# Performance work log

Measured on AMD Instinct MI355X. Metric: run time of the kernel, lower is better.

The kernel has to match this reference:

```python
import jax, jax.numpy as jnp
import numpy as np
import math

D = 1024
H = 16
HD = D // H  # 64
SCALE = math.sqrt(HD)


def setup_inputs() -> dict:
    key = jax.random.key(0)
    ks = jax.random.split(key, 4)
    B, S = 2, 2048
    x = jax.random.normal(ks[0], (B, S, D), dtype=jnp.float32)
    attention_mask = jnp.zeros((B, S), dtype=jnp.float32)  # additive mask
    w_attn = jax.random.normal(ks[1], (D, 3 * D), dtype=jnp.float32) * (1.0 / math.sqrt(D))
    b_attn = jnp.zeros((3 * D,), dtype=jnp.float32)
    w_proj = jax.random.normal(ks[2], (D, D), dtype=jnp.float32) * (1.0 / math.sqrt(D))
    b_proj = jnp.zeros((D,), dtype=jnp.float32)
    return {"x": x, "attention_mask": attention_mask, "w_attn": w_attn,
            "b_attn": b_attn, "w_proj": w_proj, "b_proj": b_proj}


def reference(x, attention_mask, w_attn, b_attn, w_proj, b_proj):
    B, S, _ = x.shape
    qkv = x @ w_attn + b_attn                      # [B,S,3D]
    q, k, v = jnp.split(qkv, 3, axis=-1)           # each [B,S,D]
    # split heads -> [B,H,S,HD]
    sh = lambda t: t.reshape(B, S, H, HD).transpose(0, 2, 1, 3)
    q, k, v = sh(q), sh(k), sh(v)
    scores = jnp.einsum('bhqd,bhkd->bhqk', q, k) / SCALE   # [B,H,S,S]
    scores = scores + attention_mask[:, None, None, :]      # additive mask [B,1,1,S]
    attn = jax.nn.softmax(scores, axis=-1)                  # dropout disabled (eval)
    out = jnp.einsum('bhqk,bhkd->bhqd', attn, v)            # [B,H,S,HD]
    out = out.transpose(0, 2, 1, 3).reshape(B, S, D)        # merge heads
    out = out @ w_proj + b_proj                              # resid dropout disabled
    return out
```

## Files before the change

### kernel.cpp

```cpp
#include <hip/hip_runtime.h>
#include <math.h>

#define B_  2
#define S_  2048
#define D_  1024
#define H_  16
#define HD_ 64
#define BS_ (B_ * S_)

typedef float f32x4 __attribute__((ext_vector_type(4)));
typedef int   i32x4 __attribute__((ext_vector_type(4)));

__device__ __forceinline__ float bf2f(unsigned short u) {
    union { unsigned int i; float f; } c; c.i = ((unsigned int)u) << 16; return c.f;
}
__device__ __forceinline__ unsigned short f2bf(float f) {
    union { float f; unsigned int i; } c; c.f = f;
    unsigned int r = c.i + 0x7FFFu + ((c.i >> 16) & 1u);
    return (unsigned short)(r >> 16);
}
__device__ __forceinline__ unsigned int cvtpk_bf16(float lo, float hi) {
    unsigned int r;
    asm volatile("v_cvt_pk_bf16_f32 %0, %1, %2" : "=v"(r) : "v"(lo), "v"(hi));
    return r;
}
__device__ __forceinline__ void gl_lds16(const void* g, void* l) {
    __builtin_amdgcn_global_load_lds((const __attribute__((address_space(1))) void*)g,
                                     (__attribute__((address_space(3))) void*)l, 16, 0, 0);
}
__device__ __forceinline__ void mfma_bf16(f32x4& d, i32x4 a, i32x4 b) {
    asm volatile("v_mfma_f32_16x16x32_bf16 %0, %1, %2, %0" : "+v"(d) : "v"(a), "v"(b));
}

__global__ __launch_bounds__(256) void convert_f32_bf16(
    const float* __restrict__ in, unsigned short* __restrict__ out, int n)
{
    const int i = (blockIdx.x * 256 + threadIdx.x) * 8;
    if (i >= n) return;
    const float4 a = *reinterpret_cast<const float4*>(in + i);
    const float4 b = *reinterpret_cast<const float4*>(in + i + 4);
    ushort4 u0 = make_ushort4(f2bf(a.x), f2bf(a.y), f2bf(a.z), f2bf(a.w));
    ushort4 u1 = make_ushort4(f2bf(b.x), f2bf(b.y), f2bf(b.z), f2bf(b.w));
    *reinterpret_cast<ushort4*>(out + i)     = u0;
    *reinterpret_cast<ushort4*>(out + i + 4) = u1;
}

__global__ __launch_bounds__(256) void transpose_cvt(
    const float* __restrict__ W, unsigned short* __restrict__ Wt, int K, int N)
{
    __shared__ float t[32][33];
    const int n0 = blockIdx.x * 32, k0 = blockIdx.y * 32;
    const int tx = threadIdx.x & 31, ty = threadIdx.x >> 5;
#pragma unroll
    for (int r = 0; r < 32; r += 8)
        t[ty + r][tx] = W[(size_t)(k0 + ty + r) * N + n0 + tx];
    __syncthreads();
#pragma unroll
    for (int r = 0; r < 32; r += 8)
        Wt[(size_t)(n0 + ty + r) * K + k0 + tx] = f2bf(t[tx][ty + r]);
}

template <typename OutT>
__global__ __launch_bounds__(256) void gemm_bt_bf16(
    const unsigned short* __restrict__ A,
    const unsigned short* __restrict__ Bt,
    const float* __restrict__ bias,
    OutT* __restrict__ C, int M, int N, int K)
{
    __shared__ alignas(16) unsigned short As[4096];
    __shared__ alignas(16) unsigned short Bs[4096];

    const int tid  = threadIdx.x;
    const int wave = tid >> 6;
    const int l    = tid & 63;
    const int g    = l >> 4;
    const int r    = l & 15;
    const int wr   = wave >> 1, wc = wave & 1;
    const int row0 = blockIdx.y * 128;
    const int col0 = blockIdx.x * 128;

    const size_t aoff0 = (size_t)(row0 +   0 + l) * K + wave * 8;
    const size_t aoff1 = (size_t)(row0 +  64 + l) * K + wave * 8;
    const size_t boff0 = (size_t)(col0 +   0 + l) * K + wave * 8;
    const size_t boff1 = (size_t)(col0 +  64 + l) * K + wave * 8;

    f32x4 acc[4][4];
#pragma unroll
    for (int mi = 0; mi < 4; ++mi)
#pragma unroll
        for (int ni = 0; ni < 4; ++ni) acc[mi][ni] = (f32x4)0.f;

    for (int kt = 0; kt < K; kt += 32) {
        __syncthreads();
        gl_lds16(A  + aoff0 + kt, As + wave * 1024);
        gl_lds16(A  + aoff1 + kt, As + wave * 1024 + 512);
        gl_lds16(Bt + boff0 + kt, Bs + wave * 1024);
        gl_lds16(Bt + boff1 + kt, Bs + wave * 1024 + 512);
        __syncthreads();

        const unsigned short* Ab = As + g * 1024;
        const unsigned short* Bb = Bs + g * 1024;
        i32x4 af[4], bf[4];
#pragma unroll
        for (int mi = 0; mi < 4; ++mi)
            af[mi] = *reinterpret_cast<const i32x4*>(Ab + (wr * 64 + mi * 16 + r) * 8);
#pragma unroll
        for (int ni = 0; ni < 4; ++ni)
            bf[ni] = *reinterpret_cast<const i32x4*>(Bb + (wc * 64 + ni * 16 + r) * 8);
#pragma unroll
        for (int mi = 0; mi < 4; ++mi)
#pragma unroll
            for (int ni = 0; ni < 4; ++ni)
                mfma_bf16(acc[mi][ni], af[mi], bf[ni]);
    }

#pragma unroll
    for (int ni = 0; ni < 4; ++ni) {
        const int n = col0 + wc * 64 + ni * 16 + r;
        const float bv = bias[n];
#pragma unroll
        for (int mi = 0; mi < 4; ++mi) {
#pragma unroll
            for (int e = 0; e < 4; ++e) {
                const int m = row0 + wr * 64 + mi * 16 + g * 4 + e;
                const float val = acc[mi][ni][e] + bv;
                if constexpr (sizeof(OutT) == 2)
                    C[(size_t)m * N + n] = (OutT)f2bf(val);
                else
                    C[(size_t)m * N + n] = (OutT)val;
            }
        }
    }
}

__global__ __launch_bounds__(256) void flash_attn_mfma(
    const unsigned short* __restrict__ qkv,
    const float* __restrict__ mask,
    unsigned short* __restrict__ out)
{
    __shared__ alignas(16) unsigned short Klds[64 * 64];
    __shared__ alignas(16) unsigned short Vt[64 * 64];

    const int tid  = threadIdx.x;
    const int wave = tid >> 6;
    const int l    = tid & 63;
    const int g    = l >> 4;
    const int r    = l & 15;
    const int b    = blockIdx.z;
    const int h    = blockIdx.y;
    const int q0   = blockIdx.x * 128;
    const int qw   = q0 + wave * 32;

    const size_t rs = 3 * (size_t)D_;
    const unsigned short* qb = qkv + (size_t)b * S_ * rs + (size_t)h * HD_;
    const unsigned short* kb = qb + D_;
    const unsigned short* vb = qb + 2 * D_;
    const float* mrow = mask + (size_t)b * S_;

    i32x4 qf[2][2];
#pragma unroll
    for (int ni = 0; ni < 2; ++ni)
#pragma unroll
        for (int ks = 0; ks < 2; ++ks)
            qf[ni][ks] = *reinterpret_cast<const i32x4*>(
                qb + (size_t)(qw + ni * 16 + r) * rs + ks * 32 + g * 8);

    const int kkey = wave * 16 + (l >> 3);
    const int kuni = ((l & 7) ^ ((l >> 3) & 7)) * 8;

    const int vkey  = wave * 16 + (l >> 2);
    const int vpart = l & 3;

    f32x4 acc[4][2];
    float m_i[2], l_i[2];
#pragma unroll
    for (int mi = 0; mi < 4; ++mi)
#pragma unroll
        for (int ni = 0; ni < 2; ++ni) acc[mi][ni] = (f32x4)0.f;
    m_i[0] = m_i[1] = -1e30f;
    l_i[0] = l_i[1] = 0.f;

    for (int kt = 0; kt < S_; kt += 64) {
        __syncthreads();
        gl_lds16(kb + (size_t)(kt + kkey) * rs + kuni,     Klds + wave * 1024);
        gl_lds16(kb + (size_t)(kt + kkey + 8) * rs + kuni, Klds + wave * 1024 + 512);
#pragma unroll
        for (int p = 0; p < 4; ++p) {
            const int d0 = p * 16 + vpart * 4;
            const ushort4 vv = *reinterpret_cast<const ushort4*>(
                vb + (size_t)(kt + vkey) * rs + d0);
            Vt[(d0 + 0) * 64 + (vkey ^ (((d0 + 0) & 7) << 3))] = vv.x;
            Vt[(d0 + 1) * 64 + (vkey ^ (((d0 + 1) & 7) << 3))] = vv.y;
            Vt[(d0 + 2) * 64 + (vkey ^ (((d0 + 2) & 7) << 3))] = vv.z;
            Vt[(d0 + 3) * 64 + (vkey ^ (((d0 + 3) & 7) << 3))] = vv.w;
        }
        __syncthreads();

        f32x4 s[4][2];
#pragma unroll
        for (int mi = 0; mi < 4; ++mi)
#pragma unroll
            for (int ni = 0; ni < 2; ++ni) s[mi][ni] = (f32x4)0.f;
#pragma unroll
        for (int ks = 0; ks < 2; ++ks) {
#pragma unroll
            for (int mi = 0; mi < 4; ++mi) {
                const i32x4 kf = *reinterpret_cast<const i32x4*>(
                    Klds + (mi * 16 + r) * 64 + ((ks * 32 + g * 8) ^ ((r & 7) << 3)));
#pragma unroll
                for (int ni = 0; ni < 2; ++ni)
                    mfma_bf16(s[mi][ni], kf, qf[ni][ks]);
            }
        }

#pragma unroll
        for (int mi = 0; mi < 4; ++mi) {
            const float4 mk = *reinterpret_cast<const float4*>(
                mrow + kt + mi * 16 + g * 4);
#pragma unroll
            for (int ni = 0; ni < 2; ++ni) {
                s[mi][ni][0] = s[mi][ni][0] * 0.125f + mk.x;
                s[mi][ni][1] = s[mi][ni][1] * 0.125f + mk.y;
                s[mi][ni][2] = s[mi][ni][2] * 0.125f + mk.z;
                s[mi][ni][3] = s[mi][ni][3] * 0.125f + mk.w;
            }
        }

        unsigned int pk[4][2][2];
        float corr[2];
#pragma unroll
        for (int ni = 0; ni < 2; ++ni) {
            float tmax = -1e30f;
#pragma unroll
            for (int mi = 0; mi < 4; ++mi)
#pragma unroll
                for (int e = 0; e < 4; ++e)
                    tmax = fmaxf(tmax, s[mi][ni][e]);
            tmax = fmaxf(tmax, __shfl_xor(tmax, 16));
            tmax = fmaxf(tmax, __shfl_xor(tmax, 32));
            const float mnew = fmaxf(m_i[ni], tmax);
            corr[ni] = __expf(m_i[ni] - mnew);
            m_i[ni] = mnew;
            float ls = 0.f;
#pragma unroll
            for (int mi = 0; mi < 4; ++mi) {
                float p0 = __expf(s[mi][ni][0] - mnew);
                float p1 = __expf(s[mi][ni][1] - mnew);
                float p2 = __expf(s[mi][ni][2] - mnew);
                float p3 = __expf(s[mi][ni][3] - mnew);
                ls += (p0 + p1) + (p2 + p3);
                pk[mi][ni][0] = cvtpk_bf16(p0, p1);
                pk[mi][ni][1] = cvtpk_bf16(p2, p3);
            }
            l_i[ni] = l_i[ni] * corr[ni] + ls;
#pragma unroll
            for (int mi = 0; mi < 4; ++mi) acc[mi][ni] *= corr[ni];
        }

#pragma unroll
        for (int ks = 0; ks < 2; ++ks) {
            i32x4 pf[2];
#pragma unroll
            for (int ni = 0; ni < 2; ++ni) {
#pragma unroll
                for (int w = 0; w < 4; ++w) {
                    const int src = (((g & 1) * 2 + (w >> 1)) << 4) + r;
                    const unsigned int vA = __shfl(pk[2 * ks + 0][ni][w & 1], src);
                    const unsigned int vB = __shfl(pk[2 * ks + 1][ni][w & 1], src);
                    pf[ni][w] = (int)((g >> 1) ? vB : vA);
                }
            }
#pragma unroll
            for (int mi = 0; mi < 4; ++mi) {
                const i32x4 vf = *reinterpret_cast<const i32x4*>(
                    Vt + (mi * 16 + r) * 64 + ((ks * 32 + g * 8) ^ ((r & 7) << 3)));
#pragma unroll
                for (int ni = 0; ni < 2; ++ni)
                    mfma_bf16(acc[mi][ni], vf, pf[ni]);
            }
        }
    }

#pragma unroll
    for (int ni = 0; ni < 2; ++ni) {
        float lf = l_i[ni];
        lf += __shfl_xor(lf, 16);
        lf += __shfl_xor(lf, 32);
        const float inv = 1.0f / lf;
        const size_t token = (size_t)b * S_ + qw + ni * 16 + r;
#pragma unroll
        for (int mi = 0; mi < 4; ++mi) {
            const f32x4 v = acc[mi][ni] * inv;
            uint2 w;
            w.x = cvtpk_bf16(v[0], v[1]);
            w.y = cvtpk_bf16(v[2], v[3]);
            *reinterpret_cast<uint2*>(
                out + token * D_ + h * HD_ + mi * 16 + g * 4) = w;
        }
    }
}

extern "C" void kernel_launch(void* const* d_in, const int* in_sizes, int n_in,
                              void* d_out, int out_size, void* d_ws, size_t ws_size,
                              hipStream_t stream)
{
    const float* x      = (const float*)d_in[0];
    const float* amask  = (const float*)d_in[1];
    const float* w_attn = (const float*)d_in[2];
    const float* b_attn = (const float*)d_in[3];
    const float* w_proj = (const float*)d_in[4];
    const float* b_proj = (const float*)d_in[5];
    float* out = (float*)d_out;

    unsigned short* qkvb  = (unsigned short*)d_ws;
    unsigned short* attnb = qkvb  + (size_t)BS_ * 3 * D_;
    unsigned short* xb    = attnb + (size_t)BS_ * D_;
    unsigned short* wat   = xb    + (size_t)BS_ * D_;
    unsigned short* wpt   = wat   + (size_t)3 * D_ * D_;

    convert_f32_bf16<<<(BS_ * D_) / 2048, 256, 0, stream>>>(x, xb, BS_ * D_);
    transpose_cvt<<<dim3(3 * D_ / 32, D_ / 32), 256, 0, stream>>>(w_attn, wat, D_, 3 * D_);
    transpose_cvt<<<dim3(D_ / 32, D_ / 32), 256, 0, stream>>>(w_proj, wpt, D_, D_);

    gemm_bt_bf16<unsigned short><<<dim3(3 * D_ / 128, BS_ / 128), 256, 0, stream>>>(
        xb, wat, b_attn, qkvb, BS_, 3 * D_, D_);

    flash_attn_mfma<<<dim3(S_ / 128, H_, B_), 256, 0, stream>>>(qkvb, amask, attnb);

    gemm_bt_bf16<float><<<dim3(D_ / 128, BS_ / 128), 256, 0, stream>>>(
        attnb, wpt, b_proj, out, BS_, D_, D_);
}
```

Baseline: 191.4 us.

## Split flash attention into 8 waves with 16 queries each and role-split K/V loading

The attention kernel now runs 512 threads per block, and each wave processes 16 query rows instead of 32. The first four waves load the K tile asynchronously while the other four load and transpose the V tile into LDS. The aim is more waves in flight and lower per-wave register pressure, to hide latency better. The cost is half the K/V fragment reuse per wave and more waves synchronizing on each barrier. The GEMM also gains a BN template parameter, but it is only instantiated with 128.

```diff
diff --git a/kernel.cpp b/kernel.cpp
--- a/kernel.cpp
+++ b/kernel.cpp
@@ -60,15 +60,17 @@
         Wt[(size_t)(n0 + ty + r) * K + k0 + tx] = f2bf(t[tx][ty + r]);
 }
 
-template <typename OutT>
+template <typename OutT, int BN>
 __global__ __launch_bounds__(256) void gemm_bt_bf16(
     const unsigned short* __restrict__ A,
     const unsigned short* __restrict__ Bt,
     const float* __restrict__ bias,
     OutT* __restrict__ C, int M, int N, int K)
 {
+    constexpr int NW = BN / 2;
+    constexpr int NI = NW / 16;
     __shared__ alignas(16) unsigned short As[4096];
-    __shared__ alignas(16) unsigned short Bs[4096];
+    __shared__ alignas(16) unsigned short Bs[BN * 32];
 
     const int tid  = threadIdx.x;
     const int wave = tid >> 6;
@@ -77,46 +79,50 @@
     const int r    = l & 15;
     const int wr   = wave >> 1, wc = wave & 1;
     const int row0 = blockIdx.y * 128;
-    const int col0 = blockIdx.x * 128;
+    const int col0 = blockIdx.x * BN;
 
     const size_t aoff0 = (size_t)(row0 +   0 + l) * K + wave * 8;
     const size_t aoff1 = (size_t)(row0 +  64 + l) * K + wave * 8;
     const size_t boff0 = (size_t)(col0 +   0 + l) * K + wave * 8;
     const size_t boff1 = (size_t)(col0 +  64 + l) * K + wave * 8;
 
-    f32x4 acc[4][4];
+    f32x4 acc[4][NI];
 #pragma unroll
     for (int mi = 0; mi < 4; ++mi)
 #pragma unroll
-        for (int ni = 0; ni < 4; ++ni) acc[mi][ni] = (f32x4)0.f;
+        for (int ni = 0; ni < NI; ++ni) acc[mi][ni] = (f32x4)0.f;
 
     for (int kt = 0; kt < K; kt += 32) {
         __syncthreads();
-        gl_lds16(A  + aoff0 + kt, As + wave * 1024);
-        gl_lds16(A  + aoff1 + kt, As + wave * 1024 + 512);
-        gl_lds16(Bt + boff0 + kt, Bs + wave * 1024);
-        gl_lds16(Bt + boff1 + kt, Bs + wave * 1024 + 512);
+        gl_lds16(A + aoff0 + kt, As + wave * 1024);
+        gl_lds16(A + aoff1 + kt, As + wave * 1024 + 512);
+        if constexpr (BN == 128) {
+            gl_lds16(Bt + boff0 + kt, Bs + wave * 1024);
+            gl_lds16(Bt + boff1 + kt, Bs + wave * 1024 + 512);
+        } else {
+            gl_lds16(Bt + boff0 + kt, Bs + wave * 512);
+        }
         __syncthreads();
 
         const unsigned short* Ab = As + g * 1024;
-        const unsigned short* Bb = Bs + g * 1024;
-        i32x4 af[4], bf[4];
+        const unsigned short* Bb = Bs + g * (BN * 8);
+        i32x4 af[4], bf[NI];
 #pragma unroll
         for (int mi = 0; mi < 4; ++mi)
             af[mi] = *reinterpret_cast<const i32x4*>(Ab + (wr * 64 + mi * 16 + r) * 8);
 #pragma unroll
-        for (int ni = 0; ni < 4; ++ni)
-            bf[ni] = *reinterpret_cast<const i32x4*>(Bb + (wc * 64 + ni * 16 + r) * 8);
+        for (int ni = 0; ni < NI; ++ni)
+            bf[ni] = *reinterpret_cast<const i32x4*>(Bb + (wc * NW + ni * 16 + r) * 8);
 #pragma unroll
         for (int mi = 0; mi < 4; ++mi)
 #pragma unroll
-            for (int ni = 0; ni < 4; ++ni)
+            for (int ni = 0; ni < NI; ++ni)
                 mfma_bf16(acc[mi][ni], af[mi], bf[ni]);
     }
 
 #pragma unroll
-    for (int ni = 0; ni < 4; ++ni) {
-        const int n = col0 + wc * 64 + ni * 16 + r;
+    for (int ni = 0; ni < NI; ++ni) {
+        const int n = col0 + wc * NW + ni * 16 + r;
         const float bv = bias[n];
 #pragma unroll
         for (int mi = 0; mi < 4; ++mi) {
@@ -133,7 +139,7 @@
     }
 }
 
-__global__ __launch_bounds__(256) void flash_attn_mfma(
+__global__ __launch_bounds__(512) void flash_attn_mfma(
     const unsigned short* __restrict__ qkv,
     const float* __restrict__ mask,
     unsigned short* __restrict__ out)
@@ -149,7 +155,7 @@
     const int b    = blockIdx.z;
     const int h    = blockIdx.y;
     const int q0   = blockIdx.x * 128;
-    const int qw   = q0 + wave * 32;
+    const int qw   = q0 + wave * 16;
 
     const size_t rs = 3 * (size_t)D_;
     const unsigned short* qb = qkv + (size_t)b * S_ * rs + (size_t)h * HD_;
@@ -157,146 +163,123 @@
     const unsigned short* vb = qb + 2 * D_;
     const float* mrow = mask + (size_t)b * S_;
 
-    i32x4 qf[2][2];
-#pragma unroll
-    for (int ni = 0; ni < 2; ++ni)
-#pragma unroll
-        for (int ks = 0; ks < 2; ++ks)
-            qf[ni][ks] = *reinterpret_cast<const i32x4*>(
-                qb + (size_t)(qw + ni * 16 + r) * rs + ks * 32 + g * 8);
-
-    const int kkey = wave * 16 + (l >> 3);
-    const int kuni = ((l & 7) ^ ((l >> 3) & 7)) * 8;
-
-    const int vkey  = wave * 16 + (l >> 2);
+    i32x4 qf[2];
+#pragma unroll
+    for (int ks = 0; ks < 2; ++ks)
+        qf[ks] = *reinterpret_cast<const i32x4*>(
+            qb + (size_t)(qw + r) * rs + ks * 32 + g * 8);
+
+    const int kkey = (wave & 3) * 16 + (l >> 3);
+    const int kuni = ((l & 7) ^ (l >> 3)) * 8;
+    const int vkey = (wave & 3) * 16 + (l >> 2);
     const int vpart = l & 3;
 
-    f32x4 acc[4][2];
-    float m_i[2], l_i[2];
-#pragma unroll
-    for (int mi = 0; mi < 4; ++mi)
-#pragma unroll
-        for (int ni = 0; ni < 2; ++ni) acc[mi][ni] = (f32x4)0.f;
-    m_i[0] = m_i[1] = -1e30f;
-    l_i[0] = l_i[1] = 0.f;
+    f32x4 acc[4];
+    float m_i = -1e30f, l_i = 0.f;
+#pragma unroll
+    for (int mi = 0; mi < 4; ++mi) acc[mi] = (f32x4)0.f;
 
     for (int kt = 0; kt < S_; kt += 64) {
         __syncthreads();
-        gl_lds16(kb + (size_t)(kt + kkey) * rs + kuni,     Klds + wave * 1024);
-        gl_lds16(kb + (size_t)(kt + kkey + 8) * rs + kuni, Klds + wave * 1024 + 512);
-#pragma unroll
-        for (int p = 0; p < 4; ++p) {
-            const int d0 = p * 16 + vpart * 4;
-            const ushort4 vv = *reinterpret_cast<const ushort4*>(
-                vb + (size_t)(kt + vkey) * rs + d0);
-            Vt[(d0 + 0) * 64 + (vkey ^ (((d0 + 0) & 7) << 3))] = vv.x;
-            Vt[(d0 + 1) * 64 + (vkey ^ (((d0 + 1) & 7) << 3))] = vv.y;
-            Vt[(d0 + 2) * 64 + (vkey ^ (((d0 + 2) & 7) << 3))] = vv.z;
-            Vt[(d0 + 3) * 64 + (vkey ^ (((d0 + 3) & 7) << 3))] = vv.w;
+        if (wave < 4) {
+            gl_lds16(kb + (size_t)(kt + kkey) * rs + kuni,     Klds + wave * 1024);
+            gl_lds16(kb + (size_t)(kt + kkey + 8) * rs + kuni, Klds + wave * 1024 + 512);
+        } else {
+#pragma unroll
+            for (int p = 0; p < 4; ++p) {
+                const int d0 = p * 16 + vpart * 4;
+                const ushort4 vv = *reinterpret_cast<const ushort4*>(
+                    vb + (size_t)(kt + vkey) * rs + d0);
+                Vt[(d0 + 0) * 64 + (vkey ^ (((d0 + 0) & 7) << 3))] = vv.x;
+                Vt[(d0 + 1) * 64 + (vkey ^ (((d0 + 1) & 7) << 3))] = vv.y;
+                Vt[(d0 + 2) * 64 + (vkey ^ (((d0 + 2) & 7) << 3))] = vv.z;
+                Vt[(d0 + 3) * 64 + (vkey ^ (((d0 + 3) & 7) << 3))] = vv.w;
+            }
         }
         __syncthreads();
 
-        f32x4 s[4][2];
-#pragma unroll
-        for (int mi = 0; mi < 4; ++mi)
-#pragma unroll
-            for (int ni = 0; ni < 2; ++ni) s[mi][ni] = (f32x4)0.f;
-#pragma unroll
-        for (int ks = 0; ks < 2; ++ks) {
+        f32x4 s[4];
+#pragma unroll
+        for (int mi = 0; mi < 4; ++mi) s[mi] = (f32x4)0.f;
+#pragma unroll
+        for (int ks = 0; ks < 2; ++ks)
 #pragma unroll
             for (int mi = 0; mi < 4; ++mi) {
                 const i32x4 kf = *reinterpret_cast<const i32x4*>(
                     Klds + (mi * 16 + r) * 64 + ((ks * 32 + g * 8) ^ ((r & 7) << 3)));
-#pragma unroll
-                for (int ni = 0; ni < 2; ++ni)
-                    mfma_bf16(s[mi][ni], kf, qf[ni][ks]);
-            }
-        }
+                mfma_bf16(s[mi], kf, qf[ks]);
+            }
 
 #pragma unroll
         for (int mi = 0; mi < 4; ++mi) {
             const float4 mk = *reinterpret_cast<const float4*>(
                 mrow + kt + mi * 16 + g * 4);
-#pragma unroll
-            for (int ni = 0; ni < 2; ++ni) {
-                s[mi][ni][0] = s[mi][ni][0] * 0.125f + mk.x;
-                s[mi][ni][1] = s[mi][ni][1] * 0.125f + mk.y;
-                s[mi][ni][2] = s[mi][ni][2] * 0.125f + mk.z;
-                s[mi][ni][3] = s[mi][ni][3] * 0.125f + mk.w;
-            }
-        }
-
-        unsigned int pk[4][2][2];
-        float corr[2];
-#pragma unroll
-        for (int ni = 0; ni < 2; ++ni) {
-            float tmax = -1e30f;
-#pragma unroll
-            for (int mi = 0; mi < 4; ++mi)
-#pragma unroll
-                for (int e = 0; e < 4; ++e)
-                    tmax = fmaxf(tmax, s[mi][ni][e]);
-            tmax = fmaxf(tmax, __shfl_xor(tmax, 16));
-            tmax = fmaxf(tmax, __shfl_xor(tmax, 32));
-            const float mnew = fmaxf(m_i[ni], tmax);
-            corr[ni] = __expf(m_i[ni] - mnew);
-            m_i[ni] = mnew;
-            float ls = 0.f;
-#pragma unroll
-            for (int mi = 0; mi < 4; ++mi) {
-                float p0 = __expf(s[mi][ni][0] - mnew);
-                float p1 = __expf(s[mi][ni][1] - mnew);
-                float p2 = __expf(s[mi][ni][2] - mnew);
-                float p3 = __expf(s[mi][ni][3] - mnew);
-                ls += (p0 + p1) + (p2 + p3);
-                pk[mi][ni][0] = cvtpk_bf16(p0, p1);
-                pk[mi][ni][1] = cvtpk_bf16(p2, p3);
-            }
-            l_i[ni] = l_i[ni] * corr[ni] + ls;
-#pragma unroll
-            for (int mi = 0; mi < 4; ++mi) acc[mi][ni] *= corr[ni];
-        }
+            s[mi][0] = s[mi][0] * 0.125f + mk.x;
+            s[mi][1] = s[mi][1] * 0.125f + mk.y;
+            s[mi][2] = s[mi][2] * 0.125f + mk.z;
+            s[mi][3] = s[mi][3] * 0.125f + mk.w;
+        }
+
+        float tmax = -1e30f;
+#pragma unroll
+        for (int mi = 0; mi < 4; ++mi)
+#pragma unroll
+            for (int e = 0; e < 4; ++e)
+                tmax = fmaxf(tmax, s[mi][e]);
+        tmax = fmaxf(tmax, __shfl_xor(tmax, 16));
+        tmax = fmaxf(tmax, __shfl_xor(tmax, 32));
+        const float mnew = fmaxf(m_i, tmax);
+        const float corr = __expf(m_i - mnew);
+        m_i = mnew;
+
+        unsigned int pk[4][2];
+        float ls = 0.f;
+#pragma unroll
+        for (int mi = 0; mi < 4; ++mi) {
+            const float p0 = __expf(s[mi][0] - mnew);
+            const float p1 = __expf(s[mi][1] - mnew);
+            const float p2 = __expf(s[mi][2] - mnew);
+            const float p3 = __expf(s[mi][3] - mnew);
+            ls += (p0 + p1) + (p2 + p3);
+            pk[mi][0] = cvtpk_bf16(p0, p1);
+            pk[mi][1] = cvtpk_bf16(p2, p3);
+        }
+        l_i = l_i * corr + ls;
+#pragma unroll
+        for (int mi = 0; mi < 4; ++mi) acc[mi] *= corr;
 
 #pragma unroll
         for (int ks = 0; ks < 2; ++ks) {
-            i32x4 pf[2];
-#pragma unroll
-            for (int ni = 0; ni < 2; ++ni) {
-#pragma unroll
-                for (int w = 0; w < 4; ++w) {
-                    const int src = (((g & 1) * 2 + (w >> 1)) << 4) + r;
-                    const unsigned int vA = __shfl(pk[2 * ks + 0][ni][w & 1], src);
-                    const unsigned int vB = __shfl(pk[2 * ks + 1][ni][w & 1], src);
-                    pf[ni][w] = (int)((g >> 1) ? vB : vA);
-                }
+            i32x4 pf;
+#pragma unroll
+            for (int w = 0; w < 4; ++w) {
+                const int src = (((g & 1) * 2 + (w >> 1)) << 4) + r;
+                const unsigned int vA = __shfl(pk[2 * ks + 0][w & 1], src);
+                const unsigned int vB = __shfl(pk[2 * ks + 1][w & 1], src);
+                pf[w] = (int)((g >> 1) ? vB : vA);
             }
 #pragma unroll
             for (int mi = 0; mi < 4; ++mi) {
                 const i32x4 vf = *reinterpret_cast<const i32x4*>(
                     Vt + (mi * 16 + r) * 64 + ((ks * 32 + g * 8) ^ ((r & 7) << 3)));
-#pragma unroll
-                for (int ni = 0; ni < 2; ++ni)
-                    mfma_bf16(acc[mi][ni], vf, pf[ni]);
+                mfma_bf16(acc[mi], vf, pf);
             }
         }
     }
 
-#pragma unroll
-    for (int ni = 0; ni < 2; ++ni) {
-        float lf = l_i[ni];
-        lf += __shfl_xor(lf, 16);
-        lf += __shfl_xor(lf, 32);
-        const float inv = 1.0f / lf;
-        const size_t token = (size_t)b * S_ + qw + ni * 16 + r;
-#pragma unroll
-        for (int mi = 0; mi < 4; ++mi) {
-            const f32x4 v = acc[mi][ni] * inv;
-            uint2 w;
-            w.x = cvtpk_bf16(v[0], v[1]);
-            w.y = cvtpk_bf16(v[2], v[3]);
-            *reinterpret_cast<uint2*>(
-                out + token * D_ + h * HD_ + mi * 16 + g * 4) = w;
-        }
+    float lf = l_i;
+    lf += __shfl_xor(lf, 16);
+    lf += __shfl_xor(lf, 32);
+    const float inv = 1.0f / lf;
+    const size_t token = (size_t)b * S_ + qw + r;
+#pragma unroll
+    for (int mi = 0; mi < 4; ++mi) {
+        const f32x4 v = acc[mi] * inv;
+        uint2 w;
+        w.x = cvtpk_bf16(v[0], v[1]);
+        w.y = cvtpk_bf16(v[2], v[3]);
+        *reinterpret_cast<uint2*>(
+            out + token * D_ + h * HD_ + mi * 16 + g * 4) = w;
     }
 }
 
@@ -322,11 +305,11 @@
     transpose_cvt<<<dim3(3 * D_ / 32, D_ / 32), 256, 0, stream>>>(w_attn, wat, D_, 3 * D_);
     transpose_cvt<<<dim3(D_ / 32, D_ / 32), 256, 0, stream>>>(w_proj, wpt, D_, D_);
 
-    gemm_bt_bf16<unsigned short><<<dim3(3 * D_ / 128, BS_ / 128), 256, 0, stream>>>(
+    gemm_bt_bf16<unsigned short, 128><<<dim3(3 * D_ / 128, BS_ / 128), 256, 0, stream>>>(
         xb, wat, b_attn, qkvb, BS_, 3 * D_, D_);
 
-    flash_attn_mfma<<<dim3(S_ / 128, H_, B_), 256, 0, stream>>>(qkvb, amask, attnb);
-
-    gemm_bt_bf16<float><<<dim3(D_ / 128, BS_ / 128), 256, 0, stream>>>(
+    flash_attn_mfma<<<dim3(S_ / 128, H_, B_), 512, 0, stream>>>(qkvb, amask, attnb);
+
+    gemm_bt_bf16<float, 128><<<dim3(D_ / 128, BS_ / 128), 256, 0, stream>>>(
         attnb, wpt, b_proj, out, BS_, D_, D_);
 }
```

After: 202.0 us. 5.5% more time.
